# Optimization experiments

Hardware: AMD Instinct MI355X
Metric: run time of the kernel (lower is better)

The kernel has to match this reference:

```python
import jax, jax.numpy as jnp
import numpy as np

NV = 8192
NH = 4096

def setup_inputs() -> dict:
    key = jax.random.key(0)
    ks = jax.random.split(key, 8)
    return {
        "muvTE": jax.random.normal(ks[0], (NV,), dtype=jnp.float32),
        "varvhTE": jax.random.normal(ks[1], (NH, NV), dtype=jnp.float32),
        "varh_diagTE": jax.random.normal(ks[2], (NH,), dtype=jnp.float32),
        # strictly positive variances, bounded away from zero
        "varh_diag": jax.random.uniform(ks[3], (NH,), dtype=jnp.float32) + 0.5,
        "muh": jax.random.normal(ks[4], (NH,), dtype=jnp.float32),
        "varvh": jax.random.normal(ks[5], (NH, NV), dtype=jnp.float32),
        "muhTE": jax.random.normal(ks[6], (NH,), dtype=jnp.float32),
        "varvbarTE": jax.random.normal(ks[7], (), dtype=jnp.float32),
    }


def reference(muvTE, varvhTE, varh_diagTE, varh_diag, muh, varvh, muhTE, varvbarTE):
    nv = muvTE.shape[0]
    inv = 1.0 / varh_diag                      # diag(varh_inv), [nh]
    inv_muh = inv * muh                        # varh_inv @ muh, [nh]
    # varh_inv @ varhTE @ varh_inv @ muh  (all diagonal scalings)
    ivTEv_muh = inv * (varh_diagTE * inv_muh)  # [nh]

    # bTE: [nv]
    bTE = (muvTE
           - varvhTE.T @ inv_muh
           + varvh.T @ ivTEv_muh
           - varvh.T @ (inv * muhTE))

    # wtTE = -varh_inv varhTE varh_inv varvh + varh_inv varvhTE : [nh, nv]
    d = inv * varh_diagTE * inv                # [nh]
    wtTE = -d[:, None] * varvh + inv[:, None] * varvhTE

    # trace of sig2TEmat without materializing [nv, nv]:
    # tr(A^T diag(s) B) = sum(A * (s[:,None] * B))
    tr = (jnp.sum(varvhTE * (inv[:, None] * varvh))
          - jnp.sum(varvh * (d[:, None] * varvh))
          + jnp.sum(varvh * (inv[:, None] * varvhTE)))
    sig2TE = (varvbarTE - tr) / nv

    return (bTE, wtTE, sig2TE, muhTE, varh_diagTE)
```

## Files before the change

### kernel.cpp

```cpp
#include <hip/hip_runtime.h>

#define NV 8192
#define NH 4096
#define TPB 256
#define HPB 32
#define HCH (NH / HPB)
#define ROW4 (NV / 4)
#define VBLK (ROW4 / TPB)
#define NPART (VBLK * HCH)

typedef float f32x4 __attribute__((ext_vector_type(4)));

#define OFF_B   ((size_t)0)
#define OFF_WT  ((size_t)NV)
#define OFF_SIG ((size_t)NV + (size_t)NH * (size_t)NV)
#define OFF_MUH (OFF_SIG + 1)
#define OFF_VHD (OFF_MUH + NH)

__global__ __launch_bounds__(TPB) void init_k(
    const float* __restrict__ muvTE,
    const float* __restrict__ varh_diagTE,
    const float* __restrict__ muhTE,
    float* __restrict__ out)
{
    int i = blockIdx.x * TPB + threadIdx.x;
    if (i < NV) out[OFF_B + i] = muvTE[i];
    if (i < NH) {
        out[OFF_MUH + i] = muhTE[i];
        out[OFF_VHD + i] = varh_diagTE[i];
    }
}

__global__ __launch_bounds__(TPB) void main_k(
    const float4* __restrict__ varvhTE4,
    const float4* __restrict__ varvh4,
    const float* __restrict__ varh_diagTE,
    const float* __restrict__ varh_diag,
    const float* __restrict__ muh,
    const float* __restrict__ muhTE,
    float* __restrict__ out,
    float* __restrict__ tr_partial)
{
    __shared__ float4 coef_s[HPB];
    const int t  = threadIdx.x;
    const int h0 = blockIdx.y * HPB;

    if (t < HPB) {
        int h = h0 + t;
        float inv  = 1.0f / varh_diag[h];
        float vte  = varh_diagTE[h];
        float d    = inv * vte * inv;
        float m    = muh[h];
        coef_s[t] = make_float4(inv, inv * m, d * m - inv * muhTE[h], d);
    }
    __syncthreads();

    const int v4 = blockIdx.x * TPB + t;
    f32x4* wt4 = (f32x4*)(out + OFF_WT);

    float bx = 0.f, by = 0.f, bz = 0.f, bw = 0.f;
    float tr = 0.f;

    #pragma unroll 4
    for (int hh = 0; hh < HPB; ++hh) {
        float4 c = coef_s[hh];
        size_t idx = (size_t)(h0 + hh) * ROW4 + (size_t)v4;
        float4 aTE = varvhTE4[idx];
        float4 a   = varvh4[idx];

        f32x4 w;
        w.x = c.x * aTE.x - c.w * a.x;
        w.y = c.x * aTE.y - c.w * a.y;
        w.z = c.x * aTE.z - c.w * a.z;
        w.w = c.x * aTE.w - c.w * a.w;
        __builtin_nontemporal_store(w, &wt4[idx]);

        bx += c.z * a.x - c.y * aTE.x;
        by += c.z * a.y - c.y * aTE.y;
        bz += c.z * a.z - c.y * aTE.z;
        bw += c.z * a.w - c.y * aTE.w;

        float dot = aTE.x * a.x + aTE.y * a.y + aTE.z * a.z + aTE.w * a.w;
        float sq  = a.x * a.x + a.y * a.y + a.z * a.z + a.w * a.w;
        tr += 2.0f * c.x * dot - c.w * sq;
    }

    int v = v4 * 4;
    atomicAdd(&out[OFF_B + v + 0], bx);
    atomicAdd(&out[OFF_B + v + 1], by);
    atomicAdd(&out[OFF_B + v + 2], bz);
    atomicAdd(&out[OFF_B + v + 3], bw);

    for (int off = 32; off > 0; off >>= 1)
        tr += __shfl_down(tr, off);
    __shared__ float wsum[TPB / 64];
    if ((t & 63) == 0) wsum[t >> 6] = tr;
    __syncthreads();
    if (t == 0) {
        float s = wsum[0] + wsum[1] + wsum[2] + wsum[3];
        tr_partial[blockIdx.y * VBLK + blockIdx.x] = s;
    }
}

__global__ __launch_bounds__(TPB) void fin_k(
    const float* __restrict__ tr_partial,
    const float* __restrict__ varvbarTE,
    float* __restrict__ out)
{
    int t = threadIdx.x;
    float s = 0.f;
    for (int i = t; i < NPART; i += TPB) s += tr_partial[i];
    for (int off = 32; off > 0; off >>= 1)
        s += __shfl_down(s, off);
    __shared__ float wsum[TPB / 64];
    if ((t & 63) == 0) wsum[t >> 6] = s;
    __syncthreads();
    if (t == 0) {
        float tr = wsum[0] + wsum[1] + wsum[2] + wsum[3];
        out[OFF_SIG] = (varvbarTE[0] - tr) / (float)NV;
    }
}

extern "C" void kernel_launch(void* const* d_in, const int* in_sizes, int n_in,
                              void* d_out, int out_size, void* d_ws, size_t ws_size,
                              hipStream_t stream) {
    const float* muvTE       = (const float*)d_in[0];
    const float* varvhTE     = (const float*)d_in[1];
    const float* varh_diagTE = (const float*)d_in[2];
    const float* varh_diag   = (const float*)d_in[3];
    const float* muh         = (const float*)d_in[4];
    const float* varvh       = (const float*)d_in[5];
    const float* muhTE       = (const float*)d_in[6];
    const float* varvbarTE   = (const float*)d_in[7];
    float* out        = (float*)d_out;
    float* tr_partial = (float*)d_ws;

    init_k<<<NV / TPB, TPB, 0, stream>>>(muvTE, varh_diagTE, muhTE, out);
    main_k<<<dim3(VBLK, HCH), TPB, 0, stream>>>(
        (const float4*)varvhTE, (const float4*)varvh,
        varh_diagTE, varh_diag, muh, muhTE, out, tr_partial);
    fin_k<<<1, TPB, 0, stream>>>(tr_partial, varvbarTE, out);
}
```

Measured before the change: 354.1 us.

## Replace atomic bTE accumulation with per-chunk partials and a reduction kernel

The main kernel no longer issues float atomicAdds into bTE. Each h-chunk now writes its bTE partial vector to workspace, and a new reduction kernel sums the partials, adds muvTE and copies muhTE and varh_diagTE, which removes the init kernel. The chunk size is picked as a template parameter from the available workspace, preferring smaller chunks (more blocks), and the inner loop unroll grows to 8. The cost is extra workspace traffic (up to 256 x 32KB of partials written and read back) plus one more kernel launch.

```diff
diff --git a/kernel.cpp b/kernel.cpp
--- a/kernel.cpp
+++ b/kernel.cpp
@@ -3,11 +3,8 @@
 #define NV 8192
 #define NH 4096
 #define TPB 256
-#define HPB 32
-#define HCH (NH / HPB)
 #define ROW4 (NV / 4)
 #define VBLK (ROW4 / TPB)
-#define NPART (VBLK * HCH)
 
 typedef float f32x4 __attribute__((ext_vector_type(4)));
 
@@ -17,21 +14,9 @@
 #define OFF_MUH (OFF_SIG + 1)
 #define OFF_VHD (OFF_MUH + NH)
 
-__global__ __launch_bounds__(TPB) void init_k(
-    const float* __restrict__ muvTE,
-    const float* __restrict__ varh_diagTE,
-    const float* __restrict__ muhTE,
-    float* __restrict__ out)
-{
-    int i = blockIdx.x * TPB + threadIdx.x;
-    if (i < NV) out[OFF_B + i] = muvTE[i];
-    if (i < NH) {
-        out[OFF_MUH + i] = muhTE[i];
-        out[OFF_VHD + i] = varh_diagTE[i];
-    }
-}
 
-__global__ __launch_bounds__(TPB) void main_k(
+template <int HPB>
+__global__ __launch_bounds__(TPB) void main_t(
     const float4* __restrict__ varvhTE4,
     const float4* __restrict__ varvh4,
     const float* __restrict__ varh_diagTE,
@@ -39,18 +24,19 @@
     const float* __restrict__ muh,
     const float* __restrict__ muhTE,
     float* __restrict__ out,
-    float* __restrict__ tr_partial)
+    float* __restrict__ ws)
 {
     __shared__ float4 coef_s[HPB];
     const int t  = threadIdx.x;
-    const int h0 = blockIdx.y * HPB;
+    const int ch = blockIdx.y;
+    const int h0 = ch * HPB;
+    const int C  = NH / HPB;
 
     if (t < HPB) {
         int h = h0 + t;
-        float inv  = 1.0f / varh_diag[h];
-        float vte  = varh_diagTE[h];
-        float d    = inv * vte * inv;
-        float m    = muh[h];
+        float inv = 1.0f / varh_diag[h];
+        float d   = inv * varh_diagTE[h] * inv;
+        float m   = muh[h];
         coef_s[t] = make_float4(inv, inv * m, d * m - inv * muhTE[h], d);
     }
     __syncthreads();
@@ -61,7 +47,7 @@
     float bx = 0.f, by = 0.f, bz = 0.f, bw = 0.f;
     float tr = 0.f;
 
-    #pragma unroll 4
+    #pragma unroll 8
     for (int hh = 0; hh < HPB; ++hh) {
         float4 c = coef_s[hh];
         size_t idx = (size_t)(h0 + hh) * ROW4 + (size_t)v4;
@@ -85,31 +71,61 @@
         tr += 2.0f * c.x * dot - c.w * sq;
     }
 
-    int v = v4 * 4;
-    atomicAdd(&out[OFF_B + v + 0], bx);
-    atomicAdd(&out[OFF_B + v + 1], by);
-    atomicAdd(&out[OFF_B + v + 2], bz);
-    atomicAdd(&out[OFF_B + v + 3], bw);
+    f32x4* pb4 = (f32x4*)ws;
+    f32x4 p; p.x = bx; p.y = by; p.z = bz; p.w = bw;
+    pb4[(size_t)ch * ROW4 + v4] = p;
 
     for (int off = 32; off > 0; off >>= 1)
         tr += __shfl_down(tr, off);
     __shared__ float wsum[TPB / 64];
     if ((t & 63) == 0) wsum[t >> 6] = tr;
     __syncthreads();
-    if (t == 0) {
-        float s = wsum[0] + wsum[1] + wsum[2] + wsum[3];
-        tr_partial[blockIdx.y * VBLK + blockIdx.x] = s;
+    if (t == 0)
+        ws[(size_t)C * NV + (size_t)ch * VBLK + blockIdx.x] =
+            wsum[0] + wsum[1] + wsum[2] + wsum[3];
+}
+
+__global__ __launch_bounds__(TPB) void red_k(
+    const float* __restrict__ ws,
+    const float4* __restrict__ muv4,
+    const float* __restrict__ varh_diagTE,
+    const float* __restrict__ muhTE,
+    int C,
+    float* __restrict__ out)
+{
+    const int t  = threadIdx.x;
+    const int v4 = blockIdx.x * TPB + t;
+    const f32x4* pb4 = (const f32x4*)ws;
+
+    float4 m = muv4[v4];
+    float sx = m.x, sy = m.y, sz = m.z, sw = m.w;
+    #pragma unroll 4
+    for (int c = 0; c < C; ++c) {
+        f32x4 p = pb4[(size_t)c * ROW4 + v4];
+        sx += p.x; sy += p.y; sz += p.z; sw += p.w;
+    }
+    f32x4* ob4 = (f32x4*)(out + OFF_B);
+    f32x4 r; r.x = sx; r.y = sy; r.z = sz; r.w = sw;
+    ob4[v4] = r;
+
+    int gthreads = VBLK * TPB;
+    for (int i = blockIdx.x * TPB + t; i < NH; i += gthreads) {
+        out[OFF_MUH + i] = muhTE[i];
+        out[OFF_VHD + i] = varh_diagTE[i];
     }
 }
 
 __global__ __launch_bounds__(TPB) void fin_k(
-    const float* __restrict__ tr_partial,
+    const float* __restrict__ ws,
     const float* __restrict__ varvbarTE,
+    int C,
     float* __restrict__ out)
 {
+    const float* tr_partial = ws + (size_t)C * NV;
+    const int npart = C * VBLK;
     int t = threadIdx.x;
     float s = 0.f;
-    for (int i = t; i < NPART; i += TPB) s += tr_partial[i];
+    for (int i = t; i < npart; i += TPB) s += tr_partial[i];
     for (int off = 32; off > 0; off >>= 1)
         s += __shfl_down(s, off);
     __shared__ float wsum[TPB / 64];
@@ -119,6 +135,10 @@
         float tr = wsum[0] + wsum[1] + wsum[2] + wsum[3];
         out[OFF_SIG] = (varvbarTE[0] - tr) / (float)NV;
     }
+}
+
+static inline size_t ws_need(int C) {
+    return ((size_t)C * NV + (size_t)C * VBLK) * sizeof(float);
 }
 
 extern "C" void kernel_launch(void* const* d_in, const int* in_sizes, int n_in,
@@ -132,12 +152,32 @@
     const float* varvh       = (const float*)d_in[5];
     const float* muhTE       = (const float*)d_in[6];
     const float* varvbarTE   = (const float*)d_in[7];
-    float* out        = (float*)d_out;
-    float* tr_partial = (float*)d_ws;
+    float* out = (float*)d_out;
+    float* ws  = (float*)d_ws;
 
-    init_k<<<NV / TPB, TPB, 0, stream>>>(muvTE, varh_diagTE, muhTE, out);
-    main_k<<<dim3(VBLK, HCH), TPB, 0, stream>>>(
-        (const float4*)varvhTE, (const float4*)varvh,
-        varh_diagTE, varh_diag, muh, muhTE, out, tr_partial);
-    fin_k<<<1, TPB, 0, stream>>>(tr_partial, varvbarTE, out);
+    const float4* A = (const float4*)varvhTE;
+    const float4* B = (const float4*)varvh;
+
+    int C;
+    if (ws_size >= ws_need(256)) {
+        C = 256;
+        main_t<16><<<dim3(VBLK, C), TPB, 0, stream>>>(
+            A, B, varh_diagTE, varh_diag, muh, muhTE, out, ws);
+    } else if (ws_size >= ws_need(128)) {
+        C = 128;
+        main_t<32><<<dim3(VBLK, C), TPB, 0, stream>>>(
+            A, B, varh_diagTE, varh_diag, muh, muhTE, out, ws);
+    } else if (ws_size >= ws_need(64)) {
+        C = 64;
+        main_t<64><<<dim3(VBLK, C), TPB, 0, stream>>>(
+            A, B, varh_diagTE, varh_diag, muh, muhTE, out, ws);
+    } else {
+        C = 32;
+        main_t<128><<<dim3(VBLK, C), TPB, 0, stream>>>(
+            A, B, varh_diagTE, varh_diag, muh, muhTE, out, ws);
+    }
+
+    red_k<<<VBLK, TPB, 0, stream>>>((const float*)ws, (const float4*)muvTE,
+                                    varh_diagTE, muhTE, C, out);
+    fin_k<<<1, TPB, 0, stream>>>((const float*)ws, varvbarTE, C, out);
 }
```

Result: slower. 369.2 us (+4.3%).
